# Kernel optimization log

Measured on AMD Instinct MI355X. Metric: run time of the kernel, lower is better.

Reference implementation:

```python
import jax, jax.numpy as jnp
import numpy as np

NEG_SLOPE = 0.2
N_NODES, N_EDGES, N_FEAT, N_GRAPHS = 50000, 400000, 128, 64


def _glorot(k, shape):
    return jax.random.normal(k, shape, jnp.float32) / jnp.sqrt(jnp.float32(shape[0]))


def setup_inputs() -> dict:
    key = jax.random.key(0)
    ks = jax.random.split(key, 12)
    return {
        "x": jax.random.normal(ks[0], (N_NODES, N_FEAT), jnp.float32),
        "edge_index": jax.random.randint(ks[1], (2, N_EDGES), 0, N_NODES),
        "batch": jnp.sort(jax.random.randint(ks[2], (N_NODES,), 0, N_GRAPHS)),
        "W1": _glorot(ks[3], (N_FEAT, 64)),
        "as1": jax.random.normal(ks[4], (4, 16), jnp.float32) * 0.1,
        "ad1": jax.random.normal(ks[5], (4, 16), jnp.float32) * 0.1,
        "b1": jnp.zeros((64,), jnp.float32),
        "W2": _glorot(ks[6], (64, 256)),
        "as2": jax.random.normal(ks[7], (4, 64), jnp.float32) * 0.1,
        "ad2": jax.random.normal(ks[8], (4, 64), jnp.float32) * 0.1,
        "b2": jnp.zeros((256,), jnp.float32),
        "W3": _glorot(ks[9], (256, 512)),
        "as3": jax.random.normal(ks[10], (4, 128), jnp.float32) * 0.1,
        "ad3": jax.random.normal(ks[11], (4, 128), jnp.float32) * 0.1,
        "b3": jnp.zeros((128,), jnp.float32),
        "Wlin": _glorot(jax.random.fold_in(key, 99), (128, 10)),
        "blin": jnp.zeros((10,), jnp.float32),
    }


def _gat(x, src, dst, W, a_src, a_dst, b, concat, n):
    # PyG GATConv: per-head linear, LeakyReLU edge scores, segment softmax over
    # incoming edges of dst, weighted scatter-aggregate, then bias.
    H, C = a_src.shape
    h = (x @ W).reshape(n, H, C)                       # [N,H,C]
    es = jnp.einsum('nhc,hc->nh', h, a_src)            # score contrib of source node
    ed = jnp.einsum('nhc,hc->nh', h, a_dst)            # score contrib of target node
    e = jax.nn.leaky_relu(es[src] + ed[dst], NEG_SLOPE)  # [E,H]
    m = jax.ops.segment_max(e, dst, num_segments=n)
    m = jnp.where(jnp.isfinite(m), m, jnp.float32(0.0))
    ex = jnp.exp(e - m[dst])
    den = jax.ops.segment_sum(ex, dst, num_segments=n)
    alpha = ex / (den[dst] + jnp.float32(1e-16))       # [E,H]
    out = jax.ops.segment_sum(alpha[:, :, None] * h[src], dst, num_segments=n)  # [N,H,C]
    out = out.reshape(n, H * C) if concat else out.mean(axis=1)
    return out + b


def reference(x, edge_index, batch, W1, as1, ad1, b1, W2, as2, ad2, b2,
              W3, as3, ad3, b3, Wlin, blin):
    n = x.shape[0]
    loop = jnp.arange(n)
    src = jnp.concatenate([edge_index[0], loop])  # add self-loops (PyG default)
    dst = jnp.concatenate([edge_index[1], loop])
    h = jax.nn.elu(_gat(x, src, dst, W1, as1, ad1, b1, True, n))
    h = jax.nn.elu(_gat(h, src, dst, W2, as2, ad2, b2, True, n))
    h = jax.nn.elu(_gat(h, src, dst, W3, as3, ad3, b3, False, n))
    # global mean pool over graphs
    s = jax.ops.segment_sum(h, batch, num_segments=N_GRAPHS)
    cnt = jax.ops.segment_sum(jnp.ones((n,), h.dtype), batch, num_segments=N_GRAPHS)
    pooled = s / jnp.maximum(cnt, jnp.float32(1.0))[:, None]
    # dropout is identity in eval mode
    return pooled @ Wlin + blin
```

## Files before the change

### kernel.cpp

```cpp
#include <hip/hip_runtime.h>
#include <math.h>

#define NNODES 50000
#define NEDGES 400000
#define ETOT   (NEDGES + NNODES)
#define NGRAPHS 64

typedef _Float16 f16;
typedef _Float16 f16x4 __attribute__((ext_vector_type(4)));
typedef _Float16 f16x8 __attribute__((ext_vector_type(8)));
typedef float f32x4 __attribute__((ext_vector_type(4)));

__device__ __forceinline__ float lrelu(float x){ return x >= 0.f ? x : 0.2f*x; }
__device__ __forceinline__ float eluf(float x){ return x > 0.f ? x : expm1f(x); }

__global__ void k_one(int* __restrict__ deg){
  int i = blockIdx.x*256 + threadIdx.x;
  if (i < NNODES) deg[i] = 1;
}
__global__ void k_hist(const int* __restrict__ ei, int* __restrict__ deg){
  int e = blockIdx.x*blockDim.x + threadIdx.x;
  if (e < NEDGES) atomicAdd(&deg[ei[NEDGES + e]], 1);
}
__global__ void k_scan1(const int* __restrict__ deg, int* __restrict__ part, int n){
  __shared__ int buf[256];
  int i = blockIdx.x*256 + threadIdx.x;
  buf[threadIdx.x] = (i<n)? deg[i] : 0;
  __syncthreads();
  for (int s=128; s>0; s>>=1){ if (threadIdx.x < s) buf[threadIdx.x]+=buf[threadIdx.x+s]; __syncthreads(); }
  if (threadIdx.x==0) part[blockIdx.x]=buf[0];
}
__global__ void k_scan2(const int* __restrict__ part, int* __restrict__ bpre, int* __restrict__ row_off_last, int nb){
  __shared__ int buf[256];
  int t = threadIdx.x;
  int v = (t<nb)? part[t] : 0;
  buf[t]=v; __syncthreads();
  for (int s=1;s<256;s<<=1){ int a = (t>=s)? buf[t-s]:0; __syncthreads(); buf[t]+=a; __syncthreads(); }
  if (t<nb) bpre[t] = buf[t]-v;
  if (t==255) row_off_last[0] = buf[255];
}
__global__ void k_scan3(const int* __restrict__ deg, const int* __restrict__ bpre, int* __restrict__ row_off, int n){
  __shared__ int buf[256];
  int t = threadIdx.x;
  int i = blockIdx.x*256 + t;
  int v = (i<n)? deg[i]:0;
  buf[t]=v; __syncthreads();
  for (int s=1;s<256;s<<=1){ int a=(t>=s)?buf[t-s]:0; __syncthreads(); buf[t]+=a; __syncthreads(); }
  if (i<n) row_off[i] = bpre[blockIdx.x] + buf[t]-v;
}
__global__ void k_selfpos(const int* __restrict__ row_off, int* __restrict__ csr_src,
                          int* __restrict__ csr_dst, int* __restrict__ cursor){
  int n = blockIdx.x*256 + threadIdx.x;
  if (n < NNODES){
    int p = row_off[n];
    csr_src[p] = n; csr_dst[p] = n;
    cursor[n] = 1;
  }
}
__global__ void k_scatter(const int* __restrict__ ei, const int* __restrict__ row_off,
                          int* __restrict__ cursor, int* __restrict__ csr_src, int* __restrict__ csr_dst){
  int e = blockIdx.x*blockDim.x + threadIdx.x;
  if (e < NEDGES){
    int s = ei[e], d = ei[NEDGES+e];
    int pos = row_off[d] + atomicAdd(&cursor[d],1);
    csr_src[pos] = s; csr_dst[pos] = d;
  }
}

__global__ void k_prep(const float* __restrict__ W1, const float* __restrict__ W2, const float* __restrict__ W3,
                       const float* __restrict__ as1, const float* __restrict__ ad1,
                       const float* __restrict__ as2, const float* __restrict__ ad2,
                       const float* __restrict__ as3, const float* __restrict__ ad3,
                       f16* __restrict__ BT1, f16* __restrict__ BT2, f16* __restrict__ BT3,
                       f16* __restrict__ PT1, f16* __restrict__ PT2, f16* __restrict__ PT3){
  int u = blockIdx.x*256 + threadIdx.x;
  if (u < 8192){ int j=u>>7, k=u&127; BT1[j*128+k] = (f16)W1[(size_t)k*64+j]; return; }
  u -= 8192;
  if (u < 16384){ int col=u>>6, k=u&63; BT2[col*64+k] = (f16)W2[(size_t)k*256+col]; return; }
  u -= 16384;
  if (u < 131072){ int j=u>>10, t=u&1023, h=t>>8, k=t&255;
                   BT3[(size_t)j*1024+t] = (f16)W3[(size_t)k*512 + h*128 + j]; return; }
  u -= 131072;
  if (u < 1024){
    int o=u>>6, k=u&63; float v=0.f;
    if (o<8){ int h=o&3; if ((k>>4)==h) v = ((o<4)?as1:ad1)[h*16 + (k&15)]; }
    PT1[u] = (f16)v; return; }
  u -= 1024;
  if (u < 1024){
    int o=u>>6, k=u&63; float v=0.f;
    if (o<8){ int h=o&3;
      const float* a=((o<4)?as2:ad2)+h*64; const float* w=W2+(size_t)k*256+h*64;
      for(int c=0;c<64;c++) v=fmaf(w[c],a[c],v); }
    PT2[u] = (f16)v; return; }
  u -= 1024;
  if (u < 4096){
    int o=u>>8, k=u&255; float v=0.f;
    if (o<8){ int h=o&3;
      const float* a=((o<4)?as3:ad3)+h*128; const float* w=W3+(size_t)k*512+h*128;
      for(int c=0;c<128;c++) v=fmaf(w[c],a[c],v); }
    PT3[u] = (f16)v; }
}

__global__ void k_cvt_x(const float* __restrict__ x, f16* __restrict__ xh){
  int u = blockIdx.x*256 + threadIdx.x;
  if (u < NNODES*32){
    float4 v = *(const float4*)&x[(size_t)u*4];
    f16x4 o; o[0]=(f16)v.x; o[1]=(f16)v.y; o[2]=(f16)v.z; o[3]=(f16)v.w;
    *(f16x4*)&xh[(size_t)u*4] = o;
  }
}

template<int KF>
__global__ __launch_bounds__(256) void k_scores_m(const f16* __restrict__ g, const f16* __restrict__ PT,
                                                  float* __restrict__ esd){
  int wv = threadIdx.x>>6, lane = threadIdx.x&63;
  int r = lane&15, kb = lane>>4;
  int row0 = blockIdx.x*64 + wv*16;
  const f16* arow = g + (size_t)(row0+r)*KF + kb*8;
  const f16* brow = PT + (size_t)r*KF + kb*8;
  f32x4 acc = {0,0,0,0};
  #pragma unroll
  for (int k0=0;k0<KF;k0+=32){
    f16x8 af = *(const f16x8*)(arow + k0);
    f16x8 bf = *(const f16x8*)(brow + k0);
    acc = __builtin_amdgcn_mfma_f32_16x16x32_f16(af, bf, acc, 0,0,0);
  }
  if (r < 8){
    #pragma unroll
    for (int i=0;i<4;i++){
      int row = row0 + kb*4 + i;
      if (row < NNODES) esd[(size_t)row*8 + r] = acc[i];
    }
  }
}

__global__ __launch_bounds__(256) void k_expw(const float* __restrict__ esd, const int* __restrict__ csr_src,
                                              const int* __restrict__ csr_dst, float* __restrict__ alphaW){
  int p = blockIdx.x*256 + threadIdx.x;
  if (p >= ETOT) return;
  int s = csr_src[p], d = csr_dst[p];
  float4 a = *(const float4*)&esd[(size_t)s*8];
  float4 b = *(const float4*)&esd[(size_t)d*8+4];
  float4 r;
  r.x = expf(lrelu(a.x+b.x));
  r.y = expf(lrelu(a.y+b.y));
  r.z = expf(lrelu(a.z+b.z));
  r.w = expf(lrelu(a.w+b.w));
  *(float4*)&alphaW[(size_t)p*4] = r;
}

__global__ __launch_bounds__(256) void k_mfma_l1(const f16* __restrict__ xh, const f16* __restrict__ BT1,
                                                 f16* __restrict__ h1h){
  int wv = threadIdx.x>>6, lane = threadIdx.x&63;
  int r = lane&15, kb = lane>>4;
  int row0 = blockIdx.x*64 + wv*16;
  const f16* arow = xh + (size_t)(row0 + r)*128 + kb*8;
  f32x4 acc[4] = {{0,0,0,0},{0,0,0,0},{0,0,0,0},{0,0,0,0}};
  for (int k0=0;k0<128;k0+=32){
    f16x8 af = *(const f16x8*)(arow + k0);
    #pragma unroll
    for (int c=0;c<4;c++){
      f16x8 bf = *(const f16x8*)(BT1 + (size_t)(c*16+r)*128 + k0 + kb*8);
      acc[c] = __builtin_amdgcn_mfma_f32_16x16x32_f16(af, bf, acc[c], 0,0,0);
    }
  }
  #pragma unroll
  for (int c=0;c<4;c++)
    #pragma unroll
    for (int i=0;i<4;i++){
      int row = row0 + kb*4 + i;
      if (row < NNODES) h1h[(size_t)row*64 + c*16 + r] = (f16)acc[c][i];
    }
}

__global__ __launch_bounds__(256) void k_mfma_l2(const f16* __restrict__ agg2h, const f16* __restrict__ BT2,
                                                 const float* __restrict__ b2, f16* __restrict__ g2h){
  int wv = threadIdx.x>>6, lane = threadIdx.x&63;
  int r = lane&15, kb = lane>>4;
  int h = blockIdx.y;
  int row0 = blockIdx.x*64 + wv*16;
  const f16* arow = agg2h + (size_t)(row0 + r)*256 + h*64 + kb*8;
  f32x4 acc[4] = {{0,0,0,0},{0,0,0,0},{0,0,0,0},{0,0,0,0}};
  #pragma unroll
  for (int k0=0;k0<64;k0+=32){
    f16x8 af = *(const f16x8*)(arow + k0);
    #pragma unroll
    for (int c=0;c<4;c++){
      f16x8 bf = *(const f16x8*)(BT2 + (size_t)(h*64+c*16+r)*64 + k0 + kb*8);
      acc[c] = __builtin_amdgcn_mfma_f32_16x16x32_f16(af, bf, acc[c], 0,0,0);
    }
  }
  #pragma unroll
  for (int c=0;c<4;c++){
    int col = h*64 + c*16 + r;
    float bb = b2[col];
    #pragma unroll
    for (int i=0;i<4;i++){
      int row = row0 + kb*4 + i;
      if (row < NNODES) g2h[(size_t)row*256 + col] = (f16)eluf(acc[c][i] + bb);
    }
  }
}

__global__ __launch_bounds__(256) void k_mfma_l3(const f16* __restrict__ agg3h, const f16* __restrict__ BT3,
                                                 const float* __restrict__ b3, float* __restrict__ g3){
  int wv = threadIdx.x>>6, lane = threadIdx.x&63;
  int r = lane&15, kb = lane>>4;
  int row0 = blockIdx.x*128 + wv*32;
  const f16* a0 = agg3h + (size_t)(row0 + r)*1024 + kb*8;
  const f16* a1 = a0 + (size_t)16*1024;
  f32x4 acc[2][8];
  #pragma unroll
  for (int rt=0;rt<2;rt++)
    #pragma unroll
    for (int c=0;c<8;c++) acc[rt][c] = (f32x4){0,0,0,0};
  for (int k0=0;k0<1024;k0+=32){
    f16x8 af0 = *(const f16x8*)(a0 + k0);
    f16x8 af1 = *(const f16x8*)(a1 + k0);
    #pragma unroll
    for (int c=0;c<8;c++){
      f16x8 bf = *(const f16x8*)(BT3 + (size_t)(c*16+r)*1024 + k0 + kb*8);
      acc[0][c] = __builtin_amdgcn_mfma_f32_16x16x32_f16(af0, bf, acc[0][c], 0,0,0);
      acc[1][c] = __builtin_amdgcn_mfma_f32_16x16x32_f16(af1, bf, acc[1][c], 0,0,0);
    }
  }
  #pragma unroll
  for (int rt=0;rt<2;rt++)
    #pragma unroll
    for (int c=0;c<8;c++){
      int col = c*16 + r;
      float bb = b3[col];
      #pragma unroll
      for (int i=0;i<4;i++){
        int row = row0 + rt*16 + kb*4 + i;
        if (row < NNODES) g3[(size_t)row*128 + col] = eluf(0.25f*acc[rt][c][i] + bb);
      }
    }
}

__global__ __launch_bounds__(256) void k_gat1f(const f16* __restrict__ h1h, const float* __restrict__ alphaW,
    const int* __restrict__ row_off, const int* __restrict__ csr_src,
    const float* __restrict__ b1, f16* __restrict__ g1h){
  int n = blockIdx.x*4 + (threadIdx.x>>6);
  if (n >= NNODES) return;
  int t = threadIdx.x & 63;
  int head = t >> 4;
  int pos = row_off[n], end = row_off[n+1];
  float acc = 0.f, den = 0.f;
  for (; pos+1 < end; pos += 2){
    int s0 = csr_src[pos], s1 = csr_src[pos+1];
    float w0 = alphaW[(size_t)pos*4 + head];
    float w1 = alphaW[(size_t)(pos+1)*4 + head];
    float v0 = (float)h1h[(size_t)s0*64 + t];
    float v1 = (float)h1h[(size_t)s1*64 + t];
    acc = fmaf(w0, v0, fmaf(w1, v1, acc));
    den += w0 + w1;
  }
  if (pos < end){
    int s0 = csr_src[pos];
    float w0 = alphaW[(size_t)pos*4 + head];
    acc = fmaf(w0, (float)h1h[(size_t)s0*64 + t], acc);
    den += w0;
  }
  g1h[(size_t)n*64 + t] = (f16)eluf(acc/(den + 1e-16f) + b1[t]);
}

__global__ __launch_bounds__(256) void k_agg2f(const f16* __restrict__ g1h, const float* __restrict__ alphaW,
    const int* __restrict__ row_off, const int* __restrict__ csr_src,
    f16* __restrict__ agg2h){
  int n = blockIdx.x*4 + (threadIdx.x>>6);
  if (n >= NNODES) return;
  int t = threadIdx.x & 63;
  int pos = row_off[n], end = row_off[n+1];
  float c0=0.f,c1=0.f,c2=0.f,c3=0.f,d0=0.f,d1=0.f,d2=0.f,d3=0.f;
  for (; pos+1 < end; pos += 2){
    int s0 = csr_src[pos], s1 = csr_src[pos+1];
    float4 a = *(const float4*)&alphaW[(size_t)pos*4];
    float4 b = *(const float4*)&alphaW[(size_t)(pos+1)*4];
    float v0 = (float)g1h[(size_t)s0*64 + t];
    float v1 = (float)g1h[(size_t)s1*64 + t];
    c0=fmaf(a.x,v0,fmaf(b.x,v1,c0)); c1=fmaf(a.y,v0,fmaf(b.y,v1,c1));
    c2=fmaf(a.z,v0,fmaf(b.z,v1,c2)); c3=fmaf(a.w,v0,fmaf(b.w,v1,c3));
    d0+=a.x+b.x; d1+=a.y+b.y; d2+=a.z+b.z; d3+=a.w+b.w;
  }
  if (pos < end){
    int s0 = csr_src[pos];
    float4 a = *(const float4*)&alphaW[(size_t)pos*4];
    float v0 = (float)g1h[(size_t)s0*64 + t];
    c0=fmaf(a.x,v0,c0); c1=fmaf(a.y,v0,c1); c2=fmaf(a.z,v0,c2); c3=fmaf(a.w,v0,c3);
    d0+=a.x; d1+=a.y; d2+=a.z; d3+=a.w;
  }
  size_t base = (size_t)n*256;
  agg2h[base       + t] = (f16)(c0/(d0+1e-16f));
  agg2h[base +  64 + t] = (f16)(c1/(d1+1e-16f));
  agg2h[base + 128 + t] = (f16)(c2/(d2+1e-16f));
  agg2h[base + 192 + t] = (f16)(c3/(d3+1e-16f));
}

__global__ __launch_bounds__(256) void k_agg3f(const f16* __restrict__ g2h, const float* __restrict__ alphaW,
    const int* __restrict__ row_off, const int* __restrict__ csr_src,
    f16* __restrict__ agg3h){
  int n = blockIdx.x*4 + (threadIdx.x>>6);
  if (n >= NNODES) return;
  int lane = threadIdx.x & 63;
  int pos = row_off[n], end = row_off[n+1];
  float acc[4][4] = {};
  float d0=0.f,d1=0.f,d2=0.f,d3=0.f;
  for (; pos+1 < end; pos += 2){
    int s0 = csr_src[pos], s1 = csr_src[pos+1];
    float4 a = *(const float4*)&alphaW[(size_t)pos*4];
    float4 b = *(const float4*)&alphaW[(size_t)(pos+1)*4];
    f16x4 u0 = *(const f16x4*)&g2h[(size_t)s0*256 + lane*4];
    f16x4 u1 = *(const f16x4*)&g2h[(size_t)s1*256 + lane*4];
    float w0[4] = {a.x,a.y,a.z,a.w};
    float w1[4] = {b.x,b.y,b.z,b.w};
    #pragma unroll
    for (int h=0;h<4;h++)
      #pragma unroll
      for (int j=0;j<4;j++)
        acc[h][j] = fmaf(w0[h], (float)u0[j], fmaf(w1[h], (float)u1[j], acc[h][j]));
    d0 += a.x+b.x; d1 += a.y+b.y; d2 += a.z+b.z; d3 += a.w+b.w;
  }
  if (pos < end){
    int s0 = csr_src[pos];
    float4 a = *(const float4*)&alphaW[(size_t)pos*4];
    f16x4 u0 = *(const f16x4*)&g2h[(size_t)s0*256 + lane*4];
    float w0[4] = {a.x,a.y,a.z,a.w};
    #pragma unroll
    for (int h=0;h<4;h++)
      #pragma unroll
      for (int j=0;j<4;j++)
        acc[h][j] = fmaf(w0[h], (float)u0[j], acc[h][j]);
    d0 += a.x; d1 += a.y; d2 += a.z; d3 += a.w;
  }
  float dn[4] = {d0+1e-16f, d1+1e-16f, d2+1e-16f, d3+1e-16f};
  #pragma unroll
  for (int h=0;h<4;h++){
    f16x4 o;
    #pragma unroll
    for (int j=0;j<4;j++) o[j] = (f16)(acc[h][j]/dn[h]);
    *(f16x4*)&agg3h[(size_t)n*1024 + h*256 + lane*4] = o;
  }
}

__device__ __forceinline__ int lowerb(const int* a, int n, int v){
  int lo=0, hi=n;
  while (lo<hi){ int mid=(lo+hi)>>1; if (a[mid]<v) lo=mid+1; else hi=mid; }
  return lo;
}
__global__ void k_pool8(const float* __restrict__ g3, const int* __restrict__ batch, float* __restrict__ pooledS){
  int g = blockIdx.x, ch = blockIdx.y, c = threadIdx.x;
  int lo = lowerb(batch, NNODES, g);
  int hi = lowerb(batch, NNODES, g+1);
  int len = hi - lo;
  int b0 = lo + (len*ch)/8, b1 = lo + (len*(ch+1))/8;
  float s = 0.f;
  for (int nn=b0; nn<b1; ++nn) s += g3[(size_t)nn*128 + c];
  if (b1 > b0) atomicAdd(&pooledS[g*128+c], s);
}
__global__ void k_lin(const float* __restrict__ pooledS, const int* __restrict__ batch,
                      const float* __restrict__ Wlin, const float* __restrict__ blin, float* __restrict__ out){
  int t = threadIdx.x;
  if (t < 640){
    int g = t/10, j = t%10;
    int lo = lowerb(batch, NNODES, g);
    int hi = lowerb(batch, NNODES, g+1);
    float inv = 1.f / fmaxf((float)(hi-lo), 1.f);
    float s = blin[j];
    for (int c=0;c<128;c++) s = fmaf(pooledS[g*128+c]*inv, Wlin[c*10+j], s);
    out[t] = s;
  }
}

extern "C" void kernel_launch(void* const* d_in, const int* in_sizes, int n_in,
                              void* d_out, int out_size, void* d_ws, size_t ws_size,
                              hipStream_t stream){
  (void)in_sizes; (void)n_in; (void)out_size; (void)ws_size;
  const float* x    = (const float*)d_in[0];
  const int*   ei   = (const int*)d_in[1];
  const int*   batch= (const int*)d_in[2];
  const float* W1   = (const float*)d_in[3];
  const float* as1  = (const float*)d_in[4];
  const float* ad1  = (const float*)d_in[5];
  const float* b1   = (const float*)d_in[6];
  const float* W2   = (const float*)d_in[7];
  const float* as2  = (const float*)d_in[8];
  const float* ad2  = (const float*)d_in[9];
  const float* b2   = (const float*)d_in[10];
  const float* W3   = (const float*)d_in[11];
  const float* as3  = (const float*)d_in[12];
  const float* ad3  = (const float*)d_in[13];
  const float* b3   = (const float*)d_in[14];
  const float* Wlin = (const float*)d_in[15];
  const float* blin = (const float*)d_in[16];
  float* out = (float*)d_out;

  char* ws = (char*)d_ws;
  size_t off = 0;
  auto alloc = [&](size_t bytes)->char*{ char* p = ws + off; off += (bytes + 255) & ~(size_t)255; return p; };
  int* csr_src = (int*)alloc((size_t)ETOT*4);
  int* csr_dst = (int*)alloc((size_t)ETOT*4);
  int* row_off = (int*)alloc((size_t)(NNODES+1)*4);
  int* deg     = (int*)alloc((size_t)NNODES*4);
  int* cursor  = (int*)alloc((size_t)NNODES*4);
  int* part    = (int*)alloc(256*4);
  int* bpre    = (int*)alloc(256*4);
  float* esd   = (float*)alloc((size_t)NNODES*8*4);
  float* alphaW= (float*)alloc((size_t)ETOT*4*4);
  f16* BT1     = (f16*)alloc(8192*2);
  f16* BT2     = (f16*)alloc(16384*2);
  f16* BT3     = (f16*)alloc(131072*2);
  f16* PT1     = (f16*)alloc(1024*2);
  f16* PT2     = (f16*)alloc(1024*2);
  f16* PT3     = (f16*)alloc(4096*2);
  float* pooledS = (float*)alloc((size_t)NGRAPHS*128*4);
  f16* xh      = (f16*)alloc((size_t)NNODES*128*2);
  f16* h1h     = (f16*)alloc((size_t)NNODES*64*2);
  f16* g1h     = (f16*)alloc((size_t)NNODES*64*2);
  f16* agg2h   = (f16*)alloc((size_t)NNODES*256*2);
  f16* g2h     = (f16*)alloc((size_t)NNODES*256*2);
  f16* agg3h   = (f16*)alloc((size_t)NNODES*1024*2);
  float* g3    = (float*)alloc((size_t)NNODES*128*4);

  int nbE = (NEDGES+255)/256;
  int nbS = (NNODES+255)/256;
  int nbP = (ETOT+255)/256;
  int nb4 = (NNODES+3)/4;

  k_one<<<nbS,256,0,stream>>>(deg);
  k_hist<<<nbE,256,0,stream>>>(ei, deg);
  k_scan1<<<nbS,256,0,stream>>>(deg, part, NNODES);
  k_scan2<<<1,256,0,stream>>>(part, bpre, row_off+NNODES, nbS);
  k_scan3<<<nbS,256,0,stream>>>(deg, bpre, row_off, NNODES);
  k_selfpos<<<nbS,256,0,stream>>>(row_off, csr_src, csr_dst, cursor);
  k_scatter<<<nbE,256,0,stream>>>(ei, row_off, cursor, csr_src, csr_dst);

  k_prep<<<632,256,0,stream>>>(W1,W2,W3,as1,ad1,as2,ad2,as3,ad3,BT1,BT2,BT3,PT1,PT2,PT3);
  k_cvt_x<<<6250,256,0,stream>>>(x, xh);

  k_mfma_l1<<<782,256,0,stream>>>(xh, BT1, h1h);
  k_scores_m<64><<<782,256,0,stream>>>(h1h, PT1, esd);
  k_expw<<<nbP,256,0,stream>>>(esd, csr_src, csr_dst, alphaW);
  k_gat1f<<<nb4,256,0,stream>>>(h1h, alphaW, row_off, csr_src, b1, g1h);

  k_scores_m<64><<<782,256,0,stream>>>(g1h, PT2, esd);
  k_expw<<<nbP,256,0,stream>>>(esd, csr_src, csr_dst, alphaW);
  k_agg2f<<<nb4,256,0,stream>>>(g1h, alphaW, row_off, csr_src, agg2h);
  k_mfma_l2<<<dim3(782,4),256,0,stream>>>(agg2h, BT2, b2, g2h);

  k_scores_m<256><<<782,256,0,stream>>>(g2h, PT3, esd);
  k_expw<<<nbP,256,0,stream>>>(esd, csr_src, csr_dst, alphaW);
  k_agg3f<<<nb4,256,0,stream>>>(g2h, alphaW, row_off, csr_src, agg3h);
  k_mfma_l3<<<391,256,0,stream>>>(agg3h, BT3, b3, g3);

  hipMemsetAsync(pooledS, 0, (size_t)NGRAPHS*128*4, stream);
  k_pool8<<<dim3(NGRAPHS,8),128,0,stream>>>(g3, batch, pooledS);
  k_lin<<<1,1024,0,stream>>>(pooledS, batch, Wlin, blin, out);
}
```

Before: 411.7 us.

## Reorder layer-3 GAT to transform-then-aggregate, fusing head-mean into aggregation

Layer 3 previously aggregated the 256-wide input per head into a 1024-wide buffer and then ran a GEMM with K=1024. Now it first computes y3 = g2h @ W3 (512 wide, f16) with a K=256 GEMM, then gathers 512-wide y3 rows per edge, where each 16-lane group handles one head. The head mean, bias and ELU are fused into the aggregation through cross-lane shuffles. This cuts GEMM FLOPs and removes the 100MB agg3h intermediate, but doubles the per-edge gather width from 256 to 512 halves and stores y3 in f16, which adds rounding.

```diff
diff --git a/kernel.cpp b/kernel.cpp
--- a/kernel.cpp
+++ b/kernel.cpp
@@ -71,15 +71,15 @@
                        const float* __restrict__ as1, const float* __restrict__ ad1,
                        const float* __restrict__ as2, const float* __restrict__ ad2,
                        const float* __restrict__ as3, const float* __restrict__ ad3,
-                       f16* __restrict__ BT1, f16* __restrict__ BT2, f16* __restrict__ BT3,
+                       f16* __restrict__ BT1, f16* __restrict__ BT2, f16* __restrict__ BT3y,
                        f16* __restrict__ PT1, f16* __restrict__ PT2, f16* __restrict__ PT3){
   int u = blockIdx.x*256 + threadIdx.x;
   if (u < 8192){ int j=u>>7, k=u&127; BT1[j*128+k] = (f16)W1[(size_t)k*64+j]; return; }
   u -= 8192;
   if (u < 16384){ int col=u>>6, k=u&63; BT2[col*64+k] = (f16)W2[(size_t)k*256+col]; return; }
   u -= 16384;
-  if (u < 131072){ int j=u>>10, t=u&1023, h=t>>8, k=t&255;
-                   BT3[(size_t)j*1024+t] = (f16)W3[(size_t)k*512 + h*128 + j]; return; }
+  if (u < 131072){ int j=u>>8, k=u&255;
+                   BT3y[(size_t)j*256+k] = (f16)W3[(size_t)k*512 + j]; return; }
   u -= 131072;
   if (u < 1024){
     int o=u>>6, k=u&63; float v=0.f;
@@ -202,24 +202,25 @@
   }
 }
 
-__global__ __launch_bounds__(256) void k_mfma_l3(const f16* __restrict__ agg3h, const f16* __restrict__ BT3,
-                                                 const float* __restrict__ b3, float* __restrict__ g3){
+__global__ __launch_bounds__(256) void k_mfma_y3(const f16* __restrict__ g2h, const f16* __restrict__ BT3y,
+                                                 f16* __restrict__ y3){
   int wv = threadIdx.x>>6, lane = threadIdx.x&63;
   int r = lane&15, kb = lane>>4;
   int row0 = blockIdx.x*128 + wv*32;
-  const f16* a0 = agg3h + (size_t)(row0 + r)*1024 + kb*8;
-  const f16* a1 = a0 + (size_t)16*1024;
-  f32x4 acc[2][8];
+  int col0 = blockIdx.y*64;
+  const f16* a0 = g2h + (size_t)(row0 + r)*256 + kb*8;
+  const f16* a1 = a0 + (size_t)16*256;
+  f32x4 acc[2][4];
   #pragma unroll
   for (int rt=0;rt<2;rt++)
     #pragma unroll
-    for (int c=0;c<8;c++) acc[rt][c] = (f32x4){0,0,0,0};
-  for (int k0=0;k0<1024;k0+=32){
+    for (int c=0;c<4;c++) acc[rt][c] = (f32x4){0,0,0,0};
+  for (int k0=0;k0<256;k0+=32){
     f16x8 af0 = *(const f16x8*)(a0 + k0);
     f16x8 af1 = *(const f16x8*)(a1 + k0);
     #pragma unroll
-    for (int c=0;c<8;c++){
-      f16x8 bf = *(const f16x8*)(BT3 + (size_t)(c*16+r)*1024 + k0 + kb*8);
+    for (int c=0;c<4;c++){
+      f16x8 bf = *(const f16x8*)(BT3y + (size_t)(col0+c*16+r)*256 + k0 + kb*8);
       acc[0][c] = __builtin_amdgcn_mfma_f32_16x16x32_f16(af0, bf, acc[0][c], 0,0,0);
       acc[1][c] = __builtin_amdgcn_mfma_f32_16x16x32_f16(af1, bf, acc[1][c], 0,0,0);
     }
@@ -227,13 +228,12 @@
   #pragma unroll
   for (int rt=0;rt<2;rt++)
     #pragma unroll
-    for (int c=0;c<8;c++){
-      int col = c*16 + r;
-      float bb = b3[col];
+    for (int c=0;c<4;c++){
+      int col = col0 + c*16 + r;
       #pragma unroll
       for (int i=0;i<4;i++){
         int row = row0 + rt*16 + kb*4 + i;
-        if (row < NNODES) g3[(size_t)row*128 + col] = eluf(0.25f*acc[rt][c][i] + bb);
+        if (row < NNODES) y3[(size_t)row*512 + col] = (f16)acc[rt][c][i];
       }
     }
 }
@@ -297,49 +297,50 @@
   agg2h[base + 192 + t] = (f16)(c3/(d3+1e-16f));
 }
 
-__global__ __launch_bounds__(256) void k_agg3f(const f16* __restrict__ g2h, const float* __restrict__ alphaW,
+__global__ __launch_bounds__(256) void k_agg3y(const f16* __restrict__ y3, const float* __restrict__ alphaW,
     const int* __restrict__ row_off, const int* __restrict__ csr_src,
-    f16* __restrict__ agg3h){
+    const float* __restrict__ b3, float* __restrict__ g3){
   int n = blockIdx.x*4 + (threadIdx.x>>6);
   if (n >= NNODES) return;
   int lane = threadIdx.x & 63;
+  int head = lane >> 4;
+  int coff = lane*8;
   int pos = row_off[n], end = row_off[n+1];
-  float acc[4][4] = {};
-  float d0=0.f,d1=0.f,d2=0.f,d3=0.f;
+  float acc[8] = {};
+  float den = 0.f;
   for (; pos+1 < end; pos += 2){
     int s0 = csr_src[pos], s1 = csr_src[pos+1];
-    float4 a = *(const float4*)&alphaW[(size_t)pos*4];
-    float4 b = *(const float4*)&alphaW[(size_t)(pos+1)*4];
-    f16x4 u0 = *(const f16x4*)&g2h[(size_t)s0*256 + lane*4];
-    f16x4 u1 = *(const f16x4*)&g2h[(size_t)s1*256 + lane*4];
-    float w0[4] = {a.x,a.y,a.z,a.w};
-    float w1[4] = {b.x,b.y,b.z,b.w};
-    #pragma unroll
-    for (int h=0;h<4;h++)
-      #pragma unroll
-      for (int j=0;j<4;j++)
-        acc[h][j] = fmaf(w0[h], (float)u0[j], fmaf(w1[h], (float)u1[j], acc[h][j]));
-    d0 += a.x+b.x; d1 += a.y+b.y; d2 += a.z+b.z; d3 += a.w+b.w;
+    float w0 = alphaW[(size_t)pos*4 + head];
+    float w1 = alphaW[(size_t)(pos+1)*4 + head];
+    f16x8 u0 = *(const f16x8*)&y3[(size_t)s0*512 + coff];
+    f16x8 u1 = *(const f16x8*)&y3[(size_t)s1*512 + coff];
+    #pragma unroll
+    for (int j=0;j<8;j++)
+      acc[j] = fmaf(w0, (float)u0[j], fmaf(w1, (float)u1[j], acc[j]));
+    den += w0 + w1;
   }
   if (pos < end){
     int s0 = csr_src[pos];
-    float4 a = *(const float4*)&alphaW[(size_t)pos*4];
-    f16x4 u0 = *(const f16x4*)&g2h[(size_t)s0*256 + lane*4];
-    float w0[4] = {a.x,a.y,a.z,a.w};
-    #pragma unroll
-    for (int h=0;h<4;h++)
-      #pragma unroll
-      for (int j=0;j<4;j++)
-        acc[h][j] = fmaf(w0[h], (float)u0[j], acc[h][j]);
-    d0 += a.x; d1 += a.y; d2 += a.z; d3 += a.w;
-  }
-  float dn[4] = {d0+1e-16f, d1+1e-16f, d2+1e-16f, d3+1e-16f};
-  #pragma unroll
-  for (int h=0;h<4;h++){
-    f16x4 o;
-    #pragma unroll
-    for (int j=0;j<4;j++) o[j] = (f16)(acc[h][j]/dn[h]);
-    *(f16x4*)&agg3h[(size_t)n*1024 + h*256 + lane*4] = o;
+    float w0 = alphaW[(size_t)pos*4 + head];
+    f16x8 u0 = *(const f16x8*)&y3[(size_t)s0*512 + coff];
+    #pragma unroll
+    for (int j=0;j<8;j++)
+      acc[j] = fmaf(w0, (float)u0[j], acc[j]);
+    den += w0;
+  }
+  float inv = 1.f/(den + 1e-16f);
+  #pragma unroll
+  for (int j=0;j<8;j++){
+    float r = acc[j]*inv;
+    r += __shfl_xor(r, 16, 64);
+    r += __shfl_xor(r, 32, 64);
+    acc[j] = r;
+  }
+  if (lane < 16){
+    int c0 = lane*8;
+    #pragma unroll
+    for (int j=0;j<8;j++)
+      g3[(size_t)n*128 + c0 + j] = eluf(0.25f*acc[j] + b3[c0+j]);
   }
 }
 
@@ -409,7 +410,7 @@
   float* alphaW= (float*)alloc((size_t)ETOT*4*4);
   f16* BT1     = (f16*)alloc(8192*2);
   f16* BT2     = (f16*)alloc(16384*2);
-  f16* BT3     = (f16*)alloc(131072*2);
+  f16* BT3y    = (f16*)alloc(131072*2);
   f16* PT1     = (f16*)alloc(1024*2);
   f16* PT2     = (f16*)alloc(1024*2);
   f16* PT3     = (f16*)alloc(4096*2);
@@ -419,7 +420,7 @@
   f16* g1h     = (f16*)alloc((size_t)NNODES*64*2);
   f16* agg2h   = (f16*)alloc((size_t)NNODES*256*2);
   f16* g2h     = (f16*)alloc((size_t)NNODES*256*2);
-  f16* agg3h   = (f16*)alloc((size_t)NNODES*1024*2);
+  f16* y3      = (f16*)alloc((size_t)NNODES*512*2);
   float* g3    = (float*)alloc((size_t)NNODES*128*4);
 
   int nbE = (NEDGES+255)/256;
@@ -435,7 +436,7 @@
   k_selfpos<<<nbS,256,0,stream>>>(row_off, csr_src, csr_dst, cursor);
   k_scatter<<<nbE,256,0,stream>>>(ei, row_off, cursor, csr_src, csr_dst);
 
-  k_prep<<<632,256,0,stream>>>(W1,W2,W3,as1,ad1,as2,ad2,as3,ad3,BT1,BT2,BT3,PT1,PT2,PT3);
+  k_prep<<<632,256,0,stream>>>(W1,W2,W3,as1,ad1,as2,ad2,as3,ad3,BT1,BT2,BT3y,PT1,PT2,PT3);
   k_cvt_x<<<6250,256,0,stream>>>(x, xh);
 
   k_mfma_l1<<<782,256,0,stream>>>(xh, BT1, h1h);
@@ -449,9 +450,9 @@
   k_mfma_l2<<<dim3(782,4),256,0,stream>>>(agg2h, BT2, b2, g2h);
 
   k_scores_m<256><<<782,256,0,stream>>>(g2h, PT3, esd);
+  k_mfma_y3<<<dim3(391,8),256,0,stream>>>(g2h, BT3y, y3);
   k_expw<<<nbP,256,0,stream>>>(esd, csr_src, csr_dst, alphaW);
-  k_agg3f<<<nb4,256,0,stream>>>(g2h, alphaW, row_off, csr_src, agg3h);
-  k_mfma_l3<<<391,256,0,stream>>>(agg3h, BT3, b3, g3);
+  k_agg3y<<<nb4,256,0,stream>>>(y3, alphaW, row_off, csr_src, b3, g3);
 
   hipMemsetAsync(pooledS, 0, (size_t)NGRAPHS*128*4, stream);
   k_pool8<<<dim3(NGRAPHS,8),128,0,stream>>>(g3, batch, pooledS);
```

Measured after the change: 420.9 us. +2.3%, slower.

## Fuse layer-1 attention scores into MFMA GEMM and unroll edge aggregation by four

Applied to the files above, without the earlier changes.

Folds the layer-1 attention projections into a per-head projected weight, PT1x, computed as W1 times a_src and a_dst. An extra MFMA inside the layer-1 GEMM kernel then writes the score buffer directly, which removes the separate layer-1 scores kernel. The three GAT aggregation loops are unrolled from two to four edges per iteration so more gathers are in flight at once. The layer-3 GEMM goes from 32 to 16 rows per wave with a doubled grid, and its aggregation buffer is aliased over dead workspace starting at xh. The aliasing relies on the workspace allocation order being exactly right, and the extra MFMA adds a small amount of work to the layer-1 GEMM.

```diff
diff --git a/kernel.cpp b/kernel.cpp
--- a/kernel.cpp
+++ b/kernel.cpp
@@ -72,20 +72,22 @@
                        const float* __restrict__ as2, const float* __restrict__ ad2,
                        const float* __restrict__ as3, const float* __restrict__ ad3,
                        f16* __restrict__ BT1, f16* __restrict__ BT2, f16* __restrict__ BT3,
-                       f16* __restrict__ PT1, f16* __restrict__ PT2, f16* __restrict__ PT3){
+                       f16* __restrict__ PT1x, f16* __restrict__ PT2, f16* __restrict__ PT3){
   int u = blockIdx.x*256 + threadIdx.x;
   if (u < 8192){ int j=u>>7, k=u&127; BT1[j*128+k] = (f16)W1[(size_t)k*64+j]; return; }
   u -= 8192;
   if (u < 16384){ int col=u>>6, k=u&63; BT2[col*64+k] = (f16)W2[(size_t)k*256+col]; return; }
   u -= 16384;
-  if (u < 131072){ int j=u>>10, t=u&1023, h=t>>8, k=t&255;
-                   BT3[(size_t)j*1024+t] = (f16)W3[(size_t)k*512 + h*128 + j]; return; }
+  if (u < 131072){ int j=u>>10, t=u&1023, h=t>>8, c=t&255;
+                   BT3[(size_t)j*1024+t] = (f16)W3[(size_t)c*512 + h*128 + j]; return; }
   u -= 131072;
-  if (u < 1024){
-    int o=u>>6, k=u&63; float v=0.f;
-    if (o<8){ int h=o&3; if ((k>>4)==h) v = ((o<4)?as1:ad1)[h*16 + (k&15)]; }
-    PT1[u] = (f16)v; return; }
-  u -= 1024;
+  if (u < 2048){
+    int o=u>>7, k=u&127; float v=0.f;
+    if (o<8){ int h=o&3;
+      const float* a=((o<4)?as1:ad1)+h*16; const float* w=W1+(size_t)k*64+h*16;
+      for(int c=0;c<16;c++) v=fmaf(w[c],a[c],v); }
+    PT1x[u] = (f16)v; return; }
+  u -= 2048;
   if (u < 1024){
     int o=u>>6, k=u&63; float v=0.f;
     if (o<8){ int h=o&3;
@@ -150,12 +152,14 @@
 }
 
 __global__ __launch_bounds__(256) void k_mfma_l1(const f16* __restrict__ xh, const f16* __restrict__ BT1,
-                                                 f16* __restrict__ h1h){
+                                                 const f16* __restrict__ PT1x,
+                                                 f16* __restrict__ h1h, float* __restrict__ esd){
   int wv = threadIdx.x>>6, lane = threadIdx.x&63;
   int r = lane&15, kb = lane>>4;
   int row0 = blockIdx.x*64 + wv*16;
   const f16* arow = xh + (size_t)(row0 + r)*128 + kb*8;
   f32x4 acc[4] = {{0,0,0,0},{0,0,0,0},{0,0,0,0},{0,0,0,0}};
+  f32x4 accs = {0,0,0,0};
   for (int k0=0;k0<128;k0+=32){
     f16x8 af = *(const f16x8*)(arow + k0);
     #pragma unroll
@@ -163,6 +167,8 @@
       f16x8 bf = *(const f16x8*)(BT1 + (size_t)(c*16+r)*128 + k0 + kb*8);
       acc[c] = __builtin_amdgcn_mfma_f32_16x16x32_f16(af, bf, acc[c], 0,0,0);
     }
+    f16x8 bs = *(const f16x8*)(PT1x + (size_t)r*128 + k0 + kb*8);
+    accs = __builtin_amdgcn_mfma_f32_16x16x32_f16(af, bs, accs, 0,0,0);
   }
   #pragma unroll
   for (int c=0;c<4;c++)
@@ -171,6 +177,13 @@
       int row = row0 + kb*4 + i;
       if (row < NNODES) h1h[(size_t)row*64 + c*16 + r] = (f16)acc[c][i];
     }
+  if (r < 8){
+    #pragma unroll
+    for (int i=0;i<4;i++){
+      int row = row0 + kb*4 + i;
+      if (row < NNODES) esd[(size_t)row*8 + r] = accs[i];
+    }
+  }
 }
 
 __global__ __launch_bounds__(256) void k_mfma_l2(const f16* __restrict__ agg2h, const f16* __restrict__ BT2,
@@ -202,40 +215,33 @@
   }
 }
 
-__global__ __launch_bounds__(256) void k_mfma_l3(const f16* __restrict__ agg3h, const f16* __restrict__ BT3,
-                                                 const float* __restrict__ b3, float* __restrict__ g3){
+__global__ __launch_bounds__(256) void k_mfma_z(const f16* __restrict__ aggz, const f16* __restrict__ BT3,
+                                                const float* __restrict__ b3, float* __restrict__ g3){
   int wv = threadIdx.x>>6, lane = threadIdx.x&63;
   int r = lane&15, kb = lane>>4;
-  int row0 = blockIdx.x*128 + wv*32;
-  const f16* a0 = agg3h + (size_t)(row0 + r)*1024 + kb*8;
-  const f16* a1 = a0 + (size_t)16*1024;
-  f32x4 acc[2][8];
-  #pragma unroll
-  for (int rt=0;rt<2;rt++)
-    #pragma unroll
-    for (int c=0;c<8;c++) acc[rt][c] = (f32x4){0,0,0,0};
+  int row0 = blockIdx.x*64 + wv*16;
+  const f16* arow = aggz + (size_t)(row0 + r)*1024 + kb*8;
+  f32x4 acc[8];
+  #pragma unroll
+  for (int c=0;c<8;c++) acc[c] = (f32x4){0,0,0,0};
   for (int k0=0;k0<1024;k0+=32){
-    f16x8 af0 = *(const f16x8*)(a0 + k0);
-    f16x8 af1 = *(const f16x8*)(a1 + k0);
+    f16x8 af = *(const f16x8*)(arow + k0);
     #pragma unroll
     for (int c=0;c<8;c++){
       f16x8 bf = *(const f16x8*)(BT3 + (size_t)(c*16+r)*1024 + k0 + kb*8);
-      acc[0][c] = __builtin_amdgcn_mfma_f32_16x16x32_f16(af0, bf, acc[0][c], 0,0,0);
-      acc[1][c] = __builtin_amdgcn_mfma_f32_16x16x32_f16(af1, bf, acc[1][c], 0,0,0);
-    }
-  }
-  #pragma unroll
-  for (int rt=0;rt<2;rt++)
-    #pragma unroll
-    for (int c=0;c<8;c++){
-      int col = c*16 + r;
-      float bb = b3[col];
-      #pragma unroll
-      for (int i=0;i<4;i++){
-        int row = row0 + rt*16 + kb*4 + i;
-        if (row < NNODES) g3[(size_t)row*128 + col] = eluf(0.25f*acc[rt][c][i] + bb);
-      }
-    }
+      acc[c] = __builtin_amdgcn_mfma_f32_16x16x32_f16(af, bf, acc[c], 0,0,0);
+    }
+  }
+  #pragma unroll
+  for (int c=0;c<8;c++){
+    int col = c*16 + r;
+    float bb = b3[col];
+    #pragma unroll
+    for (int i=0;i<4;i++){
+      int row = row0 + kb*4 + i;
+      if (row < NNODES) g3[(size_t)row*128 + col] = eluf(0.25f*acc[c][i] + bb);
+    }
+  }
 }
 
 __global__ __launch_bounds__(256) void k_gat1f(const f16* __restrict__ h1h, const float* __restrict__ alphaW,
@@ -247,16 +253,20 @@
   int head = t >> 4;
   int pos = row_off[n], end = row_off[n+1];
   float acc = 0.f, den = 0.f;
-  for (; pos+1 < end; pos += 2){
-    int s0 = csr_src[pos], s1 = csr_src[pos+1];
+  for (; pos+3 < end; pos += 4){
+    int s0 = csr_src[pos], s1 = csr_src[pos+1], s2 = csr_src[pos+2], s3 = csr_src[pos+3];
     float w0 = alphaW[(size_t)pos*4 + head];
     float w1 = alphaW[(size_t)(pos+1)*4 + head];
+    float w2 = alphaW[(size_t)(pos+2)*4 + head];
+    float w3 = alphaW[(size_t)(pos+3)*4 + head];
     float v0 = (float)h1h[(size_t)s0*64 + t];
     float v1 = (float)h1h[(size_t)s1*64 + t];
-    acc = fmaf(w0, v0, fmaf(w1, v1, acc));
-    den += w0 + w1;
-  }
-  if (pos < end){
+    float v2 = (float)h1h[(size_t)s2*64 + t];
+    float v3 = (float)h1h[(size_t)s3*64 + t];
+    acc = fmaf(w0, v0, fmaf(w1, v1, fmaf(w2, v2, fmaf(w3, v3, acc))));
+    den += (w0 + w1) + (w2 + w3);
+  }
+  for (; pos < end; ++pos){
     int s0 = csr_src[pos];
     float w0 = alphaW[(size_t)pos*4 + head];
     acc = fmaf(w0, (float)h1h[(size_t)s0*64 + t], acc);
@@ -273,17 +283,24 @@
   int t = threadIdx.x & 63;
   int pos = row_off[n], end = row_off[n+1];
   float c0=0.f,c1=0.f,c2=0.f,c3=0.f,d0=0.f,d1=0.f,d2=0.f,d3=0.f;
-  for (; pos+1 < end; pos += 2){
-    int s0 = csr_src[pos], s1 = csr_src[pos+1];
+  for (; pos+3 < end; pos += 4){
+    int s0 = csr_src[pos], s1 = csr_src[pos+1], s2 = csr_src[pos+2], s3 = csr_src[pos+3];
     float4 a = *(const float4*)&alphaW[(size_t)pos*4];
     float4 b = *(const float4*)&alphaW[(size_t)(pos+1)*4];
+    float4 c = *(const float4*)&alphaW[(size_t)(pos+2)*4];
+    float4 d = *(const float4*)&alphaW[(size_t)(pos+3)*4];
     float v0 = (float)g1h[(size_t)s0*64 + t];
     float v1 = (float)g1h[(size_t)s1*64 + t];
-    c0=fmaf(a.x,v0,fmaf(b.x,v1,c0)); c1=fmaf(a.y,v0,fmaf(b.y,v1,c1));
-    c2=fmaf(a.z,v0,fmaf(b.z,v1,c2)); c3=fmaf(a.w,v0,fmaf(b.w,v1,c3));
-    d0+=a.x+b.x; d1+=a.y+b.y; d2+=a.z+b.z; d3+=a.w+b.w;
-  }
-  if (pos < end){
+    float v2 = (float)g1h[(size_t)s2*64 + t];
+    float v3 = (float)g1h[(size_t)s3*64 + t];
+    c0=fmaf(a.x,v0,fmaf(b.x,v1,fmaf(c.x,v2,fmaf(d.x,v3,c0))));
+    c1=fmaf(a.y,v0,fmaf(b.y,v1,fmaf(c.y,v2,fmaf(d.y,v3,c1))));
+    c2=fmaf(a.z,v0,fmaf(b.z,v1,fmaf(c.z,v2,fmaf(d.z,v3,c2))));
+    c3=fmaf(a.w,v0,fmaf(b.w,v1,fmaf(c.w,v2,fmaf(d.w,v3,c3))));
+    d0+=(a.x+b.x)+(c.x+d.x); d1+=(a.y+b.y)+(c.y+d.y);
+    d2+=(a.z+b.z)+(c.z+d.z); d3+=(a.w+b.w)+(c.w+d.w);
+  }
+  for (; pos < end; ++pos){
     int s0 = csr_src[pos];
     float4 a = *(const float4*)&alphaW[(size_t)pos*4];
     float v0 = (float)g1h[(size_t)s0*64 + t];
@@ -297,40 +314,48 @@
   agg2h[base + 192 + t] = (f16)(c3/(d3+1e-16f));
 }
 
-__global__ __launch_bounds__(256) void k_agg3f(const f16* __restrict__ g2h, const float* __restrict__ alphaW,
+__global__ __launch_bounds__(256) void k_agg3n(const f16* __restrict__ g2h, const float* __restrict__ alphaW,
     const int* __restrict__ row_off, const int* __restrict__ csr_src,
-    f16* __restrict__ agg3h){
+    f16* __restrict__ aggz){
   int n = blockIdx.x*4 + (threadIdx.x>>6);
   if (n >= NNODES) return;
   int lane = threadIdx.x & 63;
   int pos = row_off[n], end = row_off[n+1];
   float acc[4][4] = {};
   float d0=0.f,d1=0.f,d2=0.f,d3=0.f;
-  for (; pos+1 < end; pos += 2){
-    int s0 = csr_src[pos], s1 = csr_src[pos+1];
+  for (; pos+3 < end; pos += 4){
+    int s0 = csr_src[pos], s1 = csr_src[pos+1], s2 = csr_src[pos+2], s3 = csr_src[pos+3];
     float4 a = *(const float4*)&alphaW[(size_t)pos*4];
     float4 b = *(const float4*)&alphaW[(size_t)(pos+1)*4];
+    float4 c = *(const float4*)&alphaW[(size_t)(pos+2)*4];
+    float4 d = *(const float4*)&alphaW[(size_t)(pos+3)*4];
     f16x4 u0 = *(const f16x4*)&g2h[(size_t)s0*256 + lane*4];
     f16x4 u1 = *(const f16x4*)&g2h[(size_t)s1*256 + lane*4];
-    float w0[4] = {a.x,a.y,a.z,a.w};
-    float w1[4] = {b.x,b.y,b.z,b.w};
+    f16x4 u2 = *(const f16x4*)&g2h[(size_t)s2*256 + lane*4];
+    f16x4 u3 = *(const f16x4*)&g2h[(size_t)s3*256 + lane*4];
+    float wa[4] = {a.x,a.y,a.z,a.w};
+    float wb[4] = {b.x,b.y,b.z,b.w};
+    float wc[4] = {c.x,c.y,c.z,c.w};
+    float wd[4] = {d.x,d.y,d.z,d.w};
     #pragma unroll
     for (int h=0;h<4;h++)
       #pragma unroll
       for (int j=0;j<4;j++)
-        acc[h][j] = fmaf(w0[h], (float)u0[j], fmaf(w1[h], (float)u1[j], acc[h][j]));
-    d0 += a.x+b.x; d1 += a.y+b.y; d2 += a.z+b.z; d3 += a.w+b.w;
-  }
-  if (pos < end){
+        acc[h][j] = fmaf(wa[h],(float)u0[j], fmaf(wb[h],(float)u1[j],
+                    fmaf(wc[h],(float)u2[j], fmaf(wd[h],(float)u3[j], acc[h][j]))));
+    d0 += (a.x+b.x)+(c.x+d.x); d1 += (a.y+b.y)+(c.y+d.y);
+    d2 += (a.z+b.z)+(c.z+d.z); d3 += (a.w+b.w)+(c.w+d.w);
+  }
+  for (; pos < end; ++pos){
     int s0 = csr_src[pos];
     float4 a = *(const float4*)&alphaW[(size_t)pos*4];
     f16x4 u0 = *(const f16x4*)&g2h[(size_t)s0*256 + lane*4];
-    float w0[4] = {a.x,a.y,a.z,a.w};
+    float wa[4] = {a.x,a.y,a.z,a.w};
     #pragma unroll
     for (int h=0;h<4;h++)
       #pragma unroll
       for (int j=0;j<4;j++)
-        acc[h][j] = fmaf(w0[h], (float)u0[j], acc[h][j]);
+        acc[h][j] = fmaf(wa[h], (float)u0[j], acc[h][j]);
     d0 += a.x; d1 += a.y; d2 += a.z; d3 += a.w;
   }
   float dn[4] = {d0+1e-16f, d1+1e-16f, d2+1e-16f, d3+1e-16f};
@@ -339,7 +364,7 @@
     f16x4 o;
     #pragma unroll
     for (int j=0;j<4;j++) o[j] = (f16)(acc[h][j]/dn[h]);
-    *(f16x4*)&agg3h[(size_t)n*1024 + h*256 + lane*4] = o;
+    *(f16x4*)&aggz[(size_t)n*1024 + h*256 + lane*4] = o;
   }
 }
 
@@ -410,17 +435,18 @@
   f16* BT1     = (f16*)alloc(8192*2);
   f16* BT2     = (f16*)alloc(16384*2);
   f16* BT3     = (f16*)alloc(131072*2);
-  f16* PT1     = (f16*)alloc(1024*2);
+  f16* PT1x    = (f16*)alloc(2048*2);
   f16* PT2     = (f16*)alloc(1024*2);
   f16* PT3     = (f16*)alloc(4096*2);
   float* pooledS = (float*)alloc((size_t)NGRAPHS*128*4);
+  f16* g2h     = (f16*)alloc((size_t)NNODES*256*2);
   f16* xh      = (f16*)alloc((size_t)NNODES*128*2);
   f16* h1h     = (f16*)alloc((size_t)NNODES*64*2);
   f16* g1h     = (f16*)alloc((size_t)NNODES*64*2);
   f16* agg2h   = (f16*)alloc((size_t)NNODES*256*2);
-  f16* g2h     = (f16*)alloc((size_t)NNODES*256*2);
-  f16* agg3h   = (f16*)alloc((size_t)NNODES*1024*2);
+  alloc((size_t)NNODES*512*2);
   float* g3    = (float*)alloc((size_t)NNODES*128*4);
+  f16* aggz    = xh;
 
   int nbE = (NEDGES+255)/256;
   int nbS = (NNODES+255)/256;
@@ -435,11 +461,10 @@
   k_selfpos<<<nbS,256,0,stream>>>(row_off, csr_src, csr_dst, cursor);
   k_scatter<<<nbE,256,0,stream>>>(ei, row_off, cursor, csr_src, csr_dst);
 
-  k_prep<<<632,256,0,stream>>>(W1,W2,W3,as1,ad1,as2,ad2,as3,ad3,BT1,BT2,BT3,PT1,PT2,PT3);
+  k_prep<<<636,256,0,stream>>>(W1,W2,W3,as1,ad1,as2,ad2,as3,ad3,BT1,BT2,BT3,PT1x,PT2,PT3);
   k_cvt_x<<<6250,256,0,stream>>>(x, xh);
 
-  k_mfma_l1<<<782,256,0,stream>>>(xh, BT1, h1h);
-  k_scores_m<64><<<782,256,0,stream>>>(h1h, PT1, esd);
+  k_mfma_l1<<<782,256,0,stream>>>(xh, BT1, PT1x, h1h, esd);
   k_expw<<<nbP,256,0,stream>>>(esd, csr_src, csr_dst, alphaW);
   k_gat1f<<<nb4,256,0,stream>>>(h1h, alphaW, row_off, csr_src, b1, g1h);
 
@@ -450,8 +475,8 @@
 
   k_scores_m<256><<<782,256,0,stream>>>(g2h, PT3, esd);
   k_expw<<<nbP,256,0,stream>>>(esd, csr_src, csr_dst, alphaW);
-  k_agg3f<<<nb4,256,0,stream>>>(g2h, alphaW, row_off, csr_src, agg3h);
-  k_mfma_l3<<<391,256,0,stream>>>(agg3h, BT3, b3, g3);
+  k_agg3n<<<nb4,256,0,stream>>>(g2h, alphaW, row_off, csr_src, aggz);
+  k_mfma_z<<<782,256,0,stream>>>(aggz, BT3, b3, g3);
 
   hipMemsetAsync(pooledS, 0, (size_t)NGRAPHS*128*4, stream);
   k_pool8<<<dim3(NGRAPHS,8),128,0,stream>>>(g3, batch, pooledS);
```

Measured after the change: 445.0 us. +8.1%, slower.
